# Performance work log

Hardware: AMD Instinct MI355X
Metric: run time of the kernel (lower is better)

The kernel has to match this reference:

```python
import jax, jax.numpy as jnp
import numpy as np

E, N, C = 8192, 512, 1024
SILU_CST = 1.6790524  # e3nn normalize2mom constant for SiLU (2nd-moment normalization)


def setup_inputs() -> dict:
    key = jax.random.key(0)
    ks = jax.random.split(key, 9)
    return {
        "edge_features": jax.random.normal(ks[0], (E, C), jnp.float32),
        "node_features": jax.random.normal(ks[1], (N, C), jnp.float32),
        "edge_index": jax.random.randint(ks[2], (2, E), 0, N),
        # GATConv params (heads=1): lin weight (no bias), att vectors, output bias
        "gat_lin_w": jax.random.normal(ks[3], (C, C), jnp.float32) / np.float32(np.sqrt(C)),
        "att_src": jax.random.normal(ks[4], (C,), jnp.float32) / np.float32(np.sqrt(C)),
        "att_dst": jax.random.normal(ks[5], (C,), jnp.float32) / np.float32(np.sqrt(C)),
        "gat_bias": jnp.zeros((C,), jnp.float32),
        # ScalarMLPFunction weights, 'uniform' init in [-sqrt(3), sqrt(3)]
        "mlp_w0": jax.random.uniform(ks[6], (C, C), jnp.float32, -np.sqrt(3), np.sqrt(3)),
        "mlp_w1": jax.random.uniform(ks[7], (C, C), jnp.float32, -np.sqrt(3), np.sqrt(3)),
    }


def _gat(x, edge_index, W, a_s, a_d, b):
    # Artificial graph: node u_e per original edge e; directed artificial edge j->i
    # iff src[j]==src[i], j<i, and neither j nor i is a self-loop edge. PyG GATConv
    # then adds self-loops for ALL E artificial nodes.
    src, dst = edge_index[0], edge_index[1]
    valid = src != dst  # self-loop removal mask on original edges
    h = x @ W                      # [E, C] shared src/dst transform (heads=1)
    al_s = h @ a_s                 # [E] alpha_src
    al_d = h @ a_d                 # [E] alpha_dst
    idx = jnp.arange(x.shape[0])
    same_src = (src[:, None] == src[None, :]) & valid[:, None] & valid[None, :]
    art = same_src & (idx[:, None] < idx[None, :])          # strict upper triangle
    mask = art | (idx[:, None] == idx[None, :])             # + GATConv self-loops
    # logits[j, i]: message from artificial node j to target i
    logits = jnp.where(mask, jax.nn.leaky_relu(al_s[:, None] + al_d[None, :], 0.2), -jnp.inf)
    alpha = jax.nn.softmax(logits, axis=0)  # softmax over sources j, per target i
    return jnp.einsum('ji,jc->ic', alpha, h) + b  # [E, C]


def _mlp(x, w0, w1):
    # ScalarMLPFunction: w scaled by norm_from_last / sqrt(h_in); silu between layers
    h = jax.nn.silu(x @ (w0 * (1.0 / np.float32(np.sqrt(C)))))
    return h @ (w1 * np.float32(SILU_CST / np.sqrt(C)))


def reference(edge_features, node_features, edge_index, gat_lin_w, att_src, att_dst,
              gat_bias, mlp_w0, mlp_w1):
    new_edge_features = _gat(edge_features, edge_index, gat_lin_w, att_src, att_dst, gat_bias)
    new_node_features = _mlp(node_features, mlp_w0, mlp_w1)
    return new_edge_features, new_node_features
```

## Files before the change

kernel.cpp:

```cpp
#include <hip/hip_runtime.h>
#include <hip/hip_bf16.h>
#include <stdint.h>

#define C_DIM 1024
#define MAXG 96
#define NSRC 512
#define NCHUNK 32

typedef __attribute__((ext_vector_type(8))) __bf16 bf16x8;
typedef __attribute__((ext_vector_type(8))) short short8;
typedef __attribute__((ext_vector_type(4))) float f32x4;

__device__ __forceinline__ short f2bf(float f) {
  unsigned u = __float_as_uint(f);
  unsigned r = (u + 0x7fffu + ((u >> 16) & 1u)) >> 16;
  return (short)r;
}
__device__ __forceinline__ float bf2f(short s) {
  return __uint_as_float(((unsigned)(unsigned short)s) << 16);
}

__device__ __forceinline__ void gload_lds16(const void* g, void* lds) {
  __builtin_amdgcn_global_load_lds(
      (const __attribute__((address_space(1))) unsigned int*)g,
      (__attribute__((address_space(3))) unsigned int*)lds,
      16, 0, 0);
}

__global__ void cvt_bf16_2(const float* __restrict__ inA, int n4A,
                           const float* __restrict__ inB, int n4B,
                           short* __restrict__ outA, short* __restrict__ outB) {
  int i = blockIdx.x * blockDim.x + threadIdx.x;
  const float* in; short* out; int j;
  if (i < n4A) { in = inA; out = outA; j = i; }
  else if (i < n4A + n4B) { in = inB; out = outB; j = i - n4A; }
  else return;
  float4 v = ((const float4*)in)[j];
  short4 o;
  o.x = f2bf(v.x); o.y = f2bf(v.y); o.z = f2bf(v.z); o.w = f2bf(v.w);
  ((short4*)out)[j] = o;
}

__global__ void transpose_cvt3(const float* __restrict__ in0, const float* __restrict__ in1,
                               const float* __restrict__ in2, short* __restrict__ out0,
                               short* __restrict__ out1, short* __restrict__ out2,
                               float s0, float s1, float s2) {
  __shared__ float tile[32][33];
  const int z = blockIdx.z;
  const float* in = z == 0 ? in0 : (z == 1 ? in1 : in2);
  short* out = z == 0 ? out0 : (z == 1 ? out1 : out2);
  const float scale = z == 0 ? s0 : (z == 1 ? s1 : s2);
  int bx = blockIdx.x * 32, by = blockIdx.y * 32;
  int x = threadIdx.x, y4 = threadIdx.y * 4;
#pragma unroll
  for (int r = 0; r < 4; ++r)
    tile[y4 + r][x] = in[(size_t)(by + y4 + r) * C_DIM + bx + x];
  __syncthreads();
#pragma unroll
  for (int r = 0; r < 4; ++r)
    out[(size_t)(bx + y4 + r) * C_DIM + by + x] = f2bf(tile[x][y4 + r] * scale);
}

template <int EPI, int BM, int BN>
__global__ __launch_bounds__(256)
void gemm_bt(const short* __restrict__ A, const short* __restrict__ Bt,
             float* __restrict__ Cf, short* __restrict__ Cb,
             int M, int N, int K, int gm ) {
  constexpr int WR = BM / 2, WC = BN / 2;
  constexpr int MT = WR / 16, NT = WC / 16;
  __shared__ __align__(16) short sA[2][BM * 64];
  __shared__ __align__(16) short sB[2][BN * 64];
  const int t = threadIdx.x;
  const int wave = t >> 6, lane = t & 63;
  const int wm = wave >> 1, wn = wave & 1;
  const int nwg = gridDim.x, q = nwg >> 3;
  const int wg = (blockIdx.x & 7) * q + (blockIdx.x >> 3);
  const int bm = wg % gm, bn = wg / gm;
  const int rm = lane & 15, kg = lane >> 4;

  f32x4 acc[MT][NT];
#pragma unroll
  for (int i = 0; i < MT; ++i)
#pragma unroll
    for (int j = 0; j < NT; ++j) acc[i][j] = f32x4{0.f, 0.f, 0.f, 0.f};

  const size_t Abase = (size_t)bm * BM * K;
  const size_t Bbase = (size_t)bn * BN * K;
  const int nk = K >> 6;

#define STAGE(kt, b)                                                             \
  {                                                                              \
    const int k0_ = (kt) << 6;                                                   \
    _Pragma("unroll") for (int i = 0; i < BM / 32; ++i) {                        \
      int c = i * 256 + t;                                                       \
      gload_lds16(A + Abase + (size_t)(c >> 3) * K + k0_ + (c & 7) * 8,          \
                  &sA[b][(i * 256 + wave * 64) * 8]);                            \
    }                                                                            \
    _Pragma("unroll") for (int i = 0; i < BN / 32; ++i) {                        \
      int c = i * 256 + t;                                                       \
      gload_lds16(Bt + Bbase + (size_t)(c >> 3) * K + k0_ + (c & 7) * 8,         \
                  &sB[b][(i * 256 + wave * 64) * 8]);                            \
    }                                                                            \
  }

  STAGE(0, 0);
  __syncthreads();

  int cb = 0;
  for (int kk = 0; kk < nk; ++kk) {
    if (kk + 1 < nk) STAGE(kk + 1, cb ^ 1);
#pragma unroll
    for (int kk2 = 0; kk2 < 2; ++kk2) {
      short8 af[MT], bfv[NT];
#pragma unroll
      for (int mt = 0; mt < MT; ++mt)
        af[mt] = *(const short8*)&sA[cb][(wm * WR + mt * 16 + rm) * 64 + kk2 * 32 + kg * 8];
#pragma unroll
      for (int nt = 0; nt < NT; ++nt)
        bfv[nt] = *(const short8*)&sB[cb][(wn * WC + nt * 16 + rm) * 64 + kk2 * 32 + kg * 8];
#pragma unroll
      for (int mt = 0; mt < MT; ++mt)
#pragma unroll
        for (int nt = 0; nt < NT; ++nt)
          acc[mt][nt] = __builtin_amdgcn_mfma_f32_16x16x32_bf16(
              __builtin_bit_cast(bf16x8, af[mt]),
              __builtin_bit_cast(bf16x8, bfv[nt]), acc[mt][nt], 0, 0, 0);
    }
    __syncthreads();
    cb ^= 1;
  }
#undef STAGE

  const int row0 = bm * BM + wm * WR;
  const int col0 = bn * BN + wn * WC;
#pragma unroll
  for (int mt = 0; mt < MT; ++mt)
#pragma unroll
    for (int nt = 0; nt < NT; ++nt) {
      f32x4 v = acc[mt][nt];
      int r0 = row0 + mt * 16 + kg * 4;
      int cc = col0 + nt * 16 + rm;
#pragma unroll
      for (int j = 0; j < 4; ++j) {
        float x = v[j];
        if (EPI == 1) {
          float s = x / (1.f + __expf(-x));
          Cb[(size_t)(r0 + j) * N + cc] = f2bf(s);
        } else if (EPI == 2) {
          Cb[(size_t)(r0 + j) * N + cc] = f2bf(x);
        } else {
          Cf[(size_t)(r0 + j) * N + cc] = x;
        }
      }
    }
}

__global__ __launch_bounds__(256)
void al_kernel(const short* __restrict__ H, const float* __restrict__ as,
               const float* __restrict__ ad, float* __restrict__ als,
               float* __restrict__ ald) {
  int row = blockIdx.x * 4 + (threadIdx.x >> 6);
  int lane = threadIdx.x & 63;
  float ss = 0.f, sd = 0.f;
  for (int q = lane * 8; q < C_DIM; q += 512) {
    short8 hv = *(const short8*)&H[(size_t)row * C_DIM + q];
#pragma unroll
    for (int j = 0; j < 8; ++j) {
      float hf = bf2f(hv[j]);
      ss += hf * as[q + j];
      sd += hf * ad[q + j];
    }
  }
#pragma unroll
  for (int off = 32; off > 0; off >>= 1) {
    ss += __shfl_down(ss, off);
    sd += __shfl_down(sd, off);
  }
  if (lane == 0) { als[row] = ss; ald[row] = sd; }
}

__global__ __launch_bounds__(256)
void group_hist(const int* __restrict__ src, const int* __restrict__ dst,
                int* __restrict__ hist) {
  __shared__ int h[NSRC];
  const int b = blockIdx.x, t = threadIdx.x;
  h[t] = 0; h[t + 256] = 0;
  __syncthreads();
  int e = b * 256 + t;
  int s = src[e];
  bool m = (s != dst[e]);
  if (m) atomicAdd(&h[s], 1);
  __syncthreads();
  hist[(size_t)t * NCHUNK + b] = h[t];
  hist[(size_t)(t + 256) * NCHUNK + b] = h[t + 256];
}

__global__ __launch_bounds__(256)
void group_scatter(const int* __restrict__ src, const int* __restrict__ dst,
                   const int* __restrict__ hist, int* __restrict__ glist,
                   int* __restrict__ epos) {
  __shared__ int ssrc[256];
  __shared__ unsigned char sval[256];
  const int b = blockIdx.x, t = threadIdx.x;
  int e = b * 256 + t;
  int s = src[e];
  bool m = (s != dst[e]);
  ssrc[t] = s;
  sval[t] = m ? 1 : 0;
  __syncthreads();
  if (!m) return;
  int p = 0;
  for (int c = 0; c < b; ++c) p += hist[(size_t)s * NCHUNK + c];
  for (int j = 0; j < t; ++j) p += (ssrc[j] == s) & sval[j];
  if (p < MAXG) { glist[s * MAXG + p] = e; epos[e] = p; }
  else epos[e] = MAXG;
}

__global__ __launch_bounds__(256)
void attn_out(const int* __restrict__ src, const int* __restrict__ dst,
              const short* __restrict__ H, const float* __restrict__ als,
              const float* __restrict__ ald, const int* __restrict__ glist,
              const int* __restrict__ epos, const float* __restrict__ bias,
              float* __restrict__ out) {
  const int i = blockIdx.x;
  const int t = threadIdx.x;
  const int s = src[i];
  const int c0 = t * 4;
  if (s == dst[i]) {
    short4 hv = *(const short4*)&H[(size_t)i * C_DIM + c0];
    float4 b4 = *(const float4*)&bias[c0];
    float4 o;
    o.x = bf2f(hv.x) + b4.x; o.y = bf2f(hv.y) + b4.y;
    o.z = bf2f(hv.z) + b4.z; o.w = bf2f(hv.w) + b4.w;
    *(float4*)&out[(size_t)i * C_DIM + c0] = o;
    return;
  }
  __shared__ int eid[MAXG + 1];
  __shared__ float ash[MAXG + 1];
  __shared__ float alv[MAXG + 1];
  const int p = epos[i];
  if (t < p) {
    int e = glist[s * MAXG + t];
    eid[t] = e;
    ash[t] = als[e];
  }
  if (t == 0) { eid[p] = i; ash[p] = als[i]; }
  __syncthreads();
  const int L = p + 1;
  const float adi = ald[i];
  float mx = -1e30f;
  for (int q = 0; q < L; ++q) {
    float x = ash[q] + adi;
    x = x > 0.f ? x : 0.2f * x;
    mx = fmaxf(mx, x);
  }
  float ssum = 0.f;
  for (int q = 0; q < L; ++q) {
    float x = ash[q] + adi;
    x = x > 0.f ? x : 0.2f * x;
    ssum += __expf(x - mx);
  }
  float rs = 1.f / ssum;
  if (t < L) {
    float x = ash[t] + adi;
    x = x > 0.f ? x : 0.2f * x;
    alv[t] = __expf(x - mx) * rs;
  }
  __syncthreads();
  float4 acc = *(const float4*)&bias[c0];
  for (int q = 0; q < L; ++q) {
    float a = alv[q];
    short4 hv = *(const short4*)&H[(size_t)eid[q] * C_DIM + c0];
    acc.x += a * bf2f(hv.x); acc.y += a * bf2f(hv.y);
    acc.z += a * bf2f(hv.z); acc.w += a * bf2f(hv.w);
  }
  *(float4*)&out[(size_t)i * C_DIM + c0] = acc;
}

extern "C" void kernel_launch(void* const* d_in, const int* in_sizes, int n_in,
                              void* d_out, int out_size, void* d_ws, size_t ws_size,
                              hipStream_t stream) {
  const float* edge_f = (const float*)d_in[0];
  const float* node_f = (const float*)d_in[1];
  const int*   eidx   = (const int*)d_in[2];
  const float* gat_w  = (const float*)d_in[3];
  const float* att_s  = (const float*)d_in[4];
  const float* att_d  = (const float*)d_in[5];
  const float* gat_b  = (const float*)d_in[6];
  const float* w0     = (const float*)d_in[7];
  const float* w1     = (const float*)d_in[8];

  const int E = in_sizes[0] / C_DIM;
  const int N = in_sizes[1] / C_DIM;
  const int* src = eidx;
  const int* dst = eidx + E;
  float* out_edge = (float*)d_out;
  float* out_node = out_edge + (size_t)E * C_DIM;

  char* ws = (char*)d_ws;
  short* Xb  = (short*)ws; ws += (size_t)E * C_DIM * 2;
  short* Wt  = (short*)ws; ws += (size_t)C_DIM * C_DIM * 2;
  short* W0t = (short*)ws; ws += (size_t)C_DIM * C_DIM * 2;
  short* W1t = (short*)ws; ws += (size_t)C_DIM * C_DIM * 2;
  short* Xnb = (short*)ws; ws += (size_t)N * C_DIM * 2;
  short* H1b = (short*)ws; ws += (size_t)N * C_DIM * 2;
  short* H   = (short*)ws; ws += (size_t)E * C_DIM * 2;
  float* ALs = (float*)ws; ws += (size_t)E * 4;
  float* ALd = (float*)ws; ws += (size_t)E * 4;
  int*   Glist = (int*)ws; ws += (size_t)NSRC * MAXG * 4;
  int*   Epos  = (int*)ws; ws += (size_t)E * 4;
  int*   Hist  = (int*)ws; ws += (size_t)NSRC * NCHUNK * 4;

  group_hist<<<dim3(NCHUNK), 256, 0, stream>>>(src, dst, Hist);
  group_scatter<<<dim3(NCHUNK), 256, 0, stream>>>(src, dst, Hist, Glist, Epos);

  const int n4e = E * C_DIM / 4, n4n = N * C_DIM / 4;
  cvt_bf16_2<<<dim3((n4e + n4n + 255) / 256), 256, 0, stream>>>(
      edge_f, n4e, node_f, n4n, Xb, Xnb);
  transpose_cvt3<<<dim3(32, 32, 3), dim3(32, 8), 0, stream>>>(
      gat_w, w0, w1, Wt, W0t, W1t, 1.0f, 0.03125f, 1.6790524f * 0.03125f);

  gemm_bt<2, 128, 128><<<dim3((E / 128) * (C_DIM / 128)), 256, 0, stream>>>(
      Xb, Wt, nullptr, H, E, C_DIM, C_DIM, E / 128);
  al_kernel<<<dim3(E / 4), 256, 0, stream>>>(H, att_s, att_d, ALs, ALd);
  attn_out<<<dim3(E), 256, 0, stream>>>(src, dst, H, ALs, ALd, Glist, Epos, gat_b, out_edge);

  gemm_bt<1, 64, 64><<<dim3((N / 64) * (C_DIM / 64)), 256, 0, stream>>>(
      Xnb, W0t, nullptr, H1b, N, C_DIM, C_DIM, N / 64);
  gemm_bt<0, 64, 64><<<dim3((N / 64) * (C_DIM / 64)), 256, 0, stream>>>(
      H1b, W1t, out_node, nullptr, N, C_DIM, C_DIM, N / 64);
}
```

Baseline: 204.9 us.

## Fuse attention logit dot products into GAT GEMM epilogue and shrink GEMM tiles

Removes the separate al_kernel pass that re-read H to compute alpha_src/alpha_dst. Each GEMM wave now computes partial dot products of its fp32 accumulators with the attention vectors, reduces them across lanes, and atomically adds them into ALs/ALd, which are zeroed in group_hist. Tile sizes are also reduced (128x128 to 64x128 for the edge GEMM, 64x64 to 32x64 for the node MLP GEMMs) to launch more workgroups. The fused logits use unrounded fp32 values rather than bf16 H, and float atomics make the summation order nondeterministic.

```diff
diff --git a/kernel.cpp b/kernel.cpp
--- a/kernel.cpp
+++ b/kernel.cpp
@@ -65,6 +65,8 @@
 __global__ __launch_bounds__(256)
 void gemm_bt(const short* __restrict__ A, const short* __restrict__ Bt,
              float* __restrict__ Cf, short* __restrict__ Cb,
+             const float* __restrict__ as, const float* __restrict__ ad,
+             float* __restrict__ als, float* __restrict__ ald,
              int M, int N, int K, int gm ) {
   constexpr int WR = BM / 2, WC = BN / 2;
   constexpr int MT = WR / 16, NT = WC / 16;
@@ -133,6 +135,16 @@
 
   const int row0 = bm * BM + wm * WR;
   const int col0 = bn * BN + wn * WC;
+
+  float as_v[NT], ad_v[NT];
+  if (EPI == 2) {
+#pragma unroll
+    for (int nt = 0; nt < NT; ++nt) {
+      as_v[nt] = as[col0 + nt * 16 + rm];
+      ad_v[nt] = ad[col0 + nt * 16 + rm];
+    }
+  }
+
 #pragma unroll
   for (int mt = 0; mt < MT; ++mt)
 #pragma unroll
@@ -153,40 +165,44 @@
         }
       }
     }
-}
-
-__global__ __launch_bounds__(256)
-void al_kernel(const short* __restrict__ H, const float* __restrict__ as,
-               const float* __restrict__ ad, float* __restrict__ als,
-               float* __restrict__ ald) {
-  int row = blockIdx.x * 4 + (threadIdx.x >> 6);
-  int lane = threadIdx.x & 63;
-  float ss = 0.f, sd = 0.f;
-  for (int q = lane * 8; q < C_DIM; q += 512) {
-    short8 hv = *(const short8*)&H[(size_t)row * C_DIM + q];
-#pragma unroll
-    for (int j = 0; j < 8; ++j) {
-      float hf = bf2f(hv[j]);
-      ss += hf * as[q + j];
-      sd += hf * ad[q + j];
-    }
-  }
-#pragma unroll
-  for (int off = 32; off > 0; off >>= 1) {
-    ss += __shfl_down(ss, off);
-    sd += __shfl_down(sd, off);
-  }
-  if (lane == 0) { als[row] = ss; ald[row] = sd; }
+
+  if (EPI == 2) {
+#pragma unroll
+    for (int mt = 0; mt < MT; ++mt)
+#pragma unroll
+      for (int j = 0; j < 4; ++j) {
+        float ps = 0.f, pd = 0.f;
+#pragma unroll
+        for (int nt = 0; nt < NT; ++nt) {
+          float x = acc[mt][nt][j];
+          ps += x * as_v[nt];
+          pd += x * ad_v[nt];
+        }
+#pragma unroll
+        for (int m = 1; m < 16; m <<= 1) {
+          ps += __shfl_xor(ps, m);
+          pd += __shfl_xor(pd, m);
+        }
+        if (rm == 0) {
+          int row = row0 + mt * 16 + kg * 4 + j;
+          atomicAdd(&als[row], ps);
+          atomicAdd(&ald[row], pd);
+        }
+      }
+  }
 }
 
 __global__ __launch_bounds__(256)
 void group_hist(const int* __restrict__ src, const int* __restrict__ dst,
-                int* __restrict__ hist) {
+                int* __restrict__ hist, float* __restrict__ als,
+                float* __restrict__ ald) {
   __shared__ int h[NSRC];
   const int b = blockIdx.x, t = threadIdx.x;
   h[t] = 0; h[t + 256] = 0;
-  __syncthreads();
   int e = b * 256 + t;
+  als[e] = 0.f;
+  ald[e] = 0.f;
+  __syncthreads();
   int s = src[e];
   bool m = (s != dst[e]);
   if (m) atomicAdd(&h[s], 1);
@@ -311,7 +327,7 @@
   int*   Epos  = (int*)ws; ws += (size_t)E * 4;
   int*   Hist  = (int*)ws; ws += (size_t)NSRC * NCHUNK * 4;
 
-  group_hist<<<dim3(NCHUNK), 256, 0, stream>>>(src, dst, Hist);
+  group_hist<<<dim3(NCHUNK), 256, 0, stream>>>(src, dst, Hist, ALs, ALd);
   group_scatter<<<dim3(NCHUNK), 256, 0, stream>>>(src, dst, Hist, Glist, Epos);
 
   const int n4e = E * C_DIM / 4, n4n = N * C_DIM / 4;
@@ -320,13 +336,12 @@
   transpose_cvt3<<<dim3(32, 32, 3), dim3(32, 8), 0, stream>>>(
       gat_w, w0, w1, Wt, W0t, W1t, 1.0f, 0.03125f, 1.6790524f * 0.03125f);
 
-  gemm_bt<2, 128, 128><<<dim3((E / 128) * (C_DIM / 128)), 256, 0, stream>>>(
-      Xb, Wt, nullptr, H, E, C_DIM, C_DIM, E / 128);
-  al_kernel<<<dim3(E / 4), 256, 0, stream>>>(H, att_s, att_d, ALs, ALd);
+  gemm_bt<2, 64, 128><<<dim3((E / 64) * (C_DIM / 128)), 256, 0, stream>>>(
+      Xb, Wt, nullptr, H, att_s, att_d, ALs, ALd, E, C_DIM, C_DIM, E / 64);
   attn_out<<<dim3(E), 256, 0, stream>>>(src, dst, H, ALs, ALd, Glist, Epos, gat_b, out_edge);
 
-  gemm_bt<1, 64, 64><<<dim3((N / 64) * (C_DIM / 64)), 256, 0, stream>>>(
-      Xnb, W0t, nullptr, H1b, N, C_DIM, C_DIM, N / 64);
-  gemm_bt<0, 64, 64><<<dim3((N / 64) * (C_DIM / 64)), 256, 0, stream>>>(
-      H1b, W1t, out_node, nullptr, N, C_DIM, C_DIM, N / 64);
-}
+  gemm_bt<1, 32, 64><<<dim3((N / 32) * (C_DIM / 64)), 256, 0, stream>>>(
+      Xnb, W0t, nullptr, H1b, nullptr, nullptr, nullptr, nullptr, N, C_DIM, C_DIM, N / 32);
+  gemm_bt<0, 32, 64><<<dim3((N / 32) * (C_DIM / 64)), 256, 0, stream>>>(
+      H1b, W1t, out_node, nullptr, nullptr, nullptr, nullptr, nullptr, N, C_DIM, C_DIM, N / 32);
+}
```

Result: slower. 212.3 us (+3.6%).
